# Performance work log

Measured on AMD Instinct MI355X. Metric: run time of the kernel, lower is better.

Reference implementation:

```python
import jax, jax.numpy as jnp
import numpy as np

H = 16        # num query heads
H_KV = 4      # num kv heads
D = 128       # head_dim
ROPE_BASE = 10000.0


def rotate_half(x):
    x1, x2 = jnp.split(x, 2, axis=-1)
    return jnp.concatenate((-x2, x1), axis=-1)


def rope_tables(T, d, dtype):
    inv_freq = 1.0 / (ROPE_BASE ** (np.arange(0, d, 2, dtype=np.float32) / d))
    t = np.arange(T, dtype=np.float32)
    freqs = np.outer(t, inv_freq)                 # [T, d/2]
    emb = np.concatenate((freqs, freqs), axis=-1)  # [T, d]
    return jnp.asarray(np.cos(emb), dtype), jnp.asarray(np.sin(emb), dtype)


def setup_inputs() -> dict:
    key = jax.random.key(0)
    ks = jax.random.split(key, 5)
    B, T, C = 2, 2048, 2048
    s = 0.02
    return {
        "x": jax.random.normal(ks[0], (B, T, C), jnp.float32),
        "wq": jax.random.normal(ks[1], (C, H * D), jnp.float32) * s,
        "wk": jax.random.normal(ks[2], (C, H_KV * D), jnp.float32) * s,
        "wv": jax.random.normal(ks[3], (C, H_KV * D), jnp.float32) * s,
        "wo": jax.random.normal(ks[4], (H * D, C), jnp.float32) * s,
    }


def reference(x, wq, wk, wv, wo):
    B, T, C = x.shape
    # QKV projections (bias=False); weights stored as [in, out]
    q = (x @ wq).reshape(B, T, H, D).transpose(0, 2, 1, 3)      # [B,H,T,D]
    k = (x @ wk).reshape(B, T, H_KV, D).transpose(0, 2, 1, 3)   # [B,Hkv,T,D]
    v = (x @ wv).reshape(B, T, H_KV, D).transpose(0, 2, 1, 3)
    # RoPE
    cos, sin = rope_tables(T, D, x.dtype)                        # [T,D]
    q = q * cos + rotate_half(q) * sin
    k = k * cos + rotate_half(k) * sin
    # GQA: repeat kv heads
    n_rep = H // H_KV
    k = jnp.repeat(k, n_rep, axis=1)                             # [B,H,T,D]
    v = jnp.repeat(v, n_rep, axis=1)
    # Causal SDPA
    scale = 1.0 / jnp.sqrt(jnp.asarray(D, x.dtype))
    att = jnp.einsum('bhqd,bhkd->bhqk', q, k) * scale            # [B,H,T,T]
    causal = jnp.tril(jnp.ones((T, T), dtype=bool))
    att = jnp.where(causal, att, jnp.asarray(-jnp.inf, x.dtype))
    att = jax.nn.softmax(att, axis=-1)
    y = jnp.einsum('bhqk,bhkd->bhqd', att, v)                    # [B,H,T,D]
    y = y.transpose(0, 2, 1, 3).reshape(B, T, H * D)
    return y @ wo
```

## Files before the change

kernel.cpp:

```cpp
#include <hip/hip_runtime.h>
#include <cstdint>
#include <cstddef>

typedef __attribute__((ext_vector_type(8))) short short8;
typedef __attribute__((ext_vector_type(4))) float f4;
typedef __attribute__((ext_vector_type(4))) unsigned int u4;

static __device__ __forceinline__ unsigned short f2bf(float x) {
  unsigned int u = __float_as_uint(x);
  unsigned int r = (u + 0x7FFFu + ((u >> 16) & 1u)) >> 16;
  return (unsigned short)r;
}

static __device__ __forceinline__ void gll16(const unsigned short* g, unsigned short* l) {
  __builtin_amdgcn_global_load_lds(
      (const __attribute__((address_space(1))) unsigned int*)g,
      (__attribute__((address_space(3))) unsigned int*)l, 16, 0, 0);
}

template <int N>
static __device__ __forceinline__ void wait_vmcnt() {
  if constexpr (N == 0) asm volatile("s_waitcnt vmcnt(0)" ::: "memory");
  else if constexpr (N == 1) asm volatile("s_waitcnt vmcnt(1)" ::: "memory");
  else if constexpr (N == 2) asm volatile("s_waitcnt vmcnt(2)" ::: "memory");
  else if constexpr (N == 3) asm volatile("s_waitcnt vmcnt(3)" ::: "memory");
  else if constexpr (N == 4) asm volatile("s_waitcnt vmcnt(4)" ::: "memory");
}

__global__ __launch_bounds__(256) void k_cvt(
    const float* __restrict__ src, unsigned short* __restrict__ dst) {
  int gid = blockIdx.x * 256 + threadIdx.x;
  const float* p = src + (size_t)gid * 8;
  f4 a = *(const f4*)p;
  f4 b = *(const f4*)(p + 4);
  union { unsigned short u[8]; u4 v; } pk;
#pragma unroll
  for (int i = 0; i < 4; ++i) { pk.u[i] = f2bf(a[i]); pk.u[4 + i] = f2bf(b[i]); }
  *(u4*)(dst + (size_t)gid * 8) = pk.v;
}

__global__ __launch_bounds__(256) void k_transpose_f(
    const float* __restrict__ src, unsigned short* __restrict__ dst, int R, int C) {
  __shared__ alignas(16) unsigned short tile[64 * 72];
  int tid = threadIdx.x;
  int c0 = blockIdx.x * 64, r0 = blockIdx.y * 64;
#pragma unroll
  for (int s = 0; s < 2; ++s) {
    int chunk = tid + s * 256;
    int c8 = chunk & 7, r = chunk >> 3;
    const float* p = src + (size_t)(r0 + r) * C + c0 + c8 * 8;
    f4 a = *(const f4*)p;
    f4 b = *(const f4*)(p + 4);
    union { unsigned short u[8]; u4 v; } pk;
#pragma unroll
    for (int i = 0; i < 4; ++i) { pk.u[i] = f2bf(a[i]); pk.u[4 + i] = f2bf(b[i]); }
    *(u4*)(tile + r * 72 + c8 * 8) = pk.v;
  }
  __syncthreads();
#pragma unroll
  for (int s = 0; s < 2; ++s) {
    int chunk = tid + s * 256;
    int r8 = chunk & 7, c = chunk >> 3;
    union { unsigned short u[8]; u4 v; } pk;
#pragma unroll
    for (int i = 0; i < 8; ++i) pk.u[i] = tile[(r8 * 8 + i) * 72 + c];
    *(u4*)(dst + (size_t)(c0 + c) * R + r0 + r8 * 8) = pk.v;
  }
}

#define PHASE(QM, QN, WAITC, ...)                                              \
  {                                                                            \
    wait_vmcnt<WAITC>();                                                       \
    __builtin_amdgcn_s_barrier();                                              \
    asm volatile("" ::: "memory");                                             \
    short8 af[FI][2], bf[2][2];                                                \
    _Pragma("unroll") for (int i = 0; i < FI; ++i)                             \
      _Pragma("unroll") for (int ks = 0; ks < 2; ++ks)                         \
        af[i][ks] = *(const short8*)(&As[cur][((QM) * (BM / 2) + wm * (BM / 4) + i * 16 + l16) * 64 + kswz[ks]]); \
    _Pragma("unroll") for (int j = 0; j < 2; ++j)                              \
      _Pragma("unroll") for (int ks = 0; ks < 2; ++ks)                         \
        bf[j][ks] = *(const short8*)(&Bs[cur][((QN) * 128 + wn * 32 + j * 16 + l16) * 64 + kswz[ks]]); \
    __VA_ARGS__                                                                \
    __builtin_amdgcn_s_setprio(1);                                             \
    _Pragma("unroll") for (int i = 0; i < FI; ++i)                             \
      _Pragma("unroll") for (int j = 0; j < 2; ++j)                            \
        _Pragma("unroll") for (int ks = 0; ks < 2; ++ks)                       \
          acc[(QM) * FI + i][(QN) * 2 + j] = __builtin_amdgcn_mfma_f32_16x16x32_bf16( \
              af[i][ks], bf[j][ks], acc[(QM) * FI + i][(QN) * 2 + j], 0, 0, 0); \
    __builtin_amdgcn_s_setprio(0);                                             \
  }

template <int BM, bool BF16OUT>
__global__ __launch_bounds__(512, 2) void k_gemm8(
    const unsigned short* __restrict__ A, const unsigned short* __restrict__ Bt,
    void* __restrict__ Cout, int M, int N, int K) {
  constexpr int CA = BM / 128;
  constexpr int FI = BM / 64;
  constexpr int WA = 2 + CA, WB = 2 * CA, WC = CA + 2, PB = CA;
  __shared__ alignas(16) unsigned short As[2][BM * 64];
  __shared__ alignas(16) unsigned short Bs[2][256 * 64];
  (void)M;

  int tid = threadIdx.x;
  int wid = tid >> 6, lane = tid & 63, quad = lane >> 4, l16 = lane & 15;
  int wm = wid >> 2, wn = wid & 3;

  int nx = gridDim.x;
  int id = blockIdx.y * nx + blockIdx.x;
  int nwg = nx * gridDim.y;
  int per = nwg >> 3;
  int lin = (id & 7) * per + (id >> 3);
  int bx = lin % nx, by = lin / nx;
  int bm = by * BM, bn = bx * 256;

  int srow = lane >> 3;
  int scol = ((lane & 7) ^ srow) << 3;
  const unsigned short* Ast = A + (size_t)(bm + wid * 8 + srow) * K + scol;
  const unsigned short* Bst = Bt + (size_t)(bn + wid * 8 + srow) * K + scol;
  const int ldsw = wid * 512;

  int kswz[2];
#pragma unroll
  for (int ks = 0; ks < 2; ++ks) kswz[ks] = (ks * 32 + quad * 8) ^ ((l16 & 7) << 3);

  f4 zero = {0.f, 0.f, 0.f, 0.f};
  f4 acc[2 * FI][4];
#pragma unroll
  for (int i = 0; i < 2 * FI; ++i)
#pragma unroll
    for (int j = 0; j < 4; ++j) acc[i][j] = zero;

  if constexpr (CA == 2) {
    gll16(Ast, &As[0][ldsw]);
    gll16(Ast + (size_t)64 * K, &As[0][ldsw + 64 * 64]);
  } else {
    gll16(Ast, &As[0][ldsw]);
  }
  gll16(Bst, &Bs[0][ldsw]);
  gll16(Bst + (size_t)64 * K, &Bs[0][ldsw + 64 * 64]);
  gll16(Bst + (size_t)128 * K, &Bs[0][ldsw + 128 * 64]);
  gll16(Bst + (size_t)192 * K, &Bs[0][ldsw + 192 * 64]);
  if constexpr (CA == 2) {
    gll16(Ast + (size_t)128 * K, &As[0][ldsw + 128 * 64]);
    gll16(Ast + (size_t)192 * K, &As[0][ldsw + 192 * 64]);
  } else {
    gll16(Ast + (size_t)64 * K, &As[0][ldsw + 64 * 64]);
  }

  int nt = K >> 6;
  int cur = 0;
  for (int t = 0; t < nt - 1; ++t) {
    int k0n = (t + 1) << 6;
    int nxt = cur ^ 1;
    unsigned short* Asn = &As[nxt][0];
    unsigned short* Bsn = &Bs[nxt][0];
    PHASE(0, 0, WA,
      if constexpr (CA == 2) {
        gll16(Ast + k0n, Asn + ldsw);
        gll16(Ast + (size_t)64 * K + k0n, Asn + ldsw + 64 * 64);
      } else {
        gll16(Ast + k0n, Asn + ldsw);
      })
    PHASE(0, 1, WB,
      gll16(Bst + k0n, Bsn + ldsw);
      gll16(Bst + (size_t)64 * K + k0n, Bsn + ldsw + 64 * 64);)
    PHASE(1, 0, WC,
      gll16(Bst + (size_t)128 * K + k0n, Bsn + ldsw + 128 * 64);
      gll16(Bst + (size_t)192 * K + k0n, Bsn + ldsw + 192 * 64);)
    PHASE(1, 1, -1,
      if constexpr (CA == 2) {
        gll16(Ast + (size_t)128 * K + k0n, Asn + ldsw + 128 * 64);
        gll16(Ast + (size_t)192 * K + k0n, Asn + ldsw + 192 * 64);
      } else {
        gll16(Ast + (size_t)64 * K + k0n, Asn + ldsw + 64 * 64);
      })
    cur = nxt;
  }
  PHASE(0, 0, WA, ;)
  PHASE(0, 1, PB, ;)
  PHASE(1, 0, 0, ;)
  PHASE(1, 1, -1, ;)

#pragma unroll
  for (int mi = 0; mi < 2 * FI; ++mi) {
    int row = bm + (mi / FI) * (BM / 2) + wm * (BM / 4) + (mi % FI) * 16 + quad * 4;
#pragma unroll
    for (int nj = 0; nj < 4; ++nj) {
      int col = bn + (nj >> 1) * 128 + wn * 32 + (nj & 1) * 16 + l16;
#pragma unroll
      for (int r = 0; r < 4; ++r) {
        if constexpr (BF16OUT)
          ((unsigned short*)Cout)[(size_t)(row + r) * N + col] = f2bf(acc[mi][nj][r]);
        else
          ((float*)Cout)[(size_t)(row + r) * N + col] = acc[mi][nj][r];
      }
    }
  }
}

__global__ __launch_bounds__(256) void k_rope(unsigned short* __restrict__ QKV) {
  int gid = blockIdx.x * 256 + threadIdx.x;
  const int TQ = 2 * 2048 * 16 * 64;
  bool isq = gid < TQ;
  int g = isq ? gid : gid - TQ;
  int d = g & 63; g >>= 6;
  int nh = isq ? 16 : 4;
  int h = g & (nh - 1); g >>= (isq ? 4 : 2);
  int t = g & 2047; int b = g >> 11;
  size_t p = (size_t)(b * 2048 + t) * 3072 + (isq ? 0 : 2048) + h * 128 + d;
  float x0 = __uint_as_float((unsigned int)QKV[p] << 16);
  float x1 = __uint_as_float((unsigned int)QKV[p + 64] << 16);
  float freq = exp2f(-(float)d * 0.20762050593046f);
  float ang = (float)t * freq;
  float cv = __cosf(ang), sv = __sinf(ang);
  float o0 = x0 * cv - x1 * sv;
  float o1 = x1 * cv + x0 * sv;
  if (isq) { o0 *= 0.088388347648318f; o1 *= 0.088388347648318f; }
  QKV[p] = f2bf(o0);
  QKV[p + 64] = f2bf(o1);
}

__global__ __launch_bounds__(256) void k_vtrans(
    const unsigned short* __restrict__ QKV, unsigned short* __restrict__ VT) {
  int gid = blockIdx.x * 256 + threadIdx.x;
  int t = gid & 2047; int g = gid >> 11;
  int d = g & 127; g >>= 7;
  int hk = g & 3; int b = g >> 2;
  VT[gid] = QKV[(size_t)(b * 2048 + t) * 3072 + 2560 + hk * 128 + d];
}

static __device__ __forceinline__ void attn_step(
    const unsigned short* __restrict__ Ks, const unsigned short* __restrict__ Vs,
    const short8* qf, f4* o, float& m, float& l,
    int quad, int l16, int qrow, int K0, bool mask) {
  f4 zero = {0.f, 0.f, 0.f, 0.f};
  f4 st[4];
#pragma unroll
  for (int kt = 0; kt < 4; ++kt) {
    st[kt] = zero;
#pragma unroll
    for (int ks = 0; ks < 4; ++ks) {
      short8 kf = *(const short8*)(Ks + (kt * 16 + l16) * 136 + ks * 32 + quad * 8);
      st[kt] = __builtin_amdgcn_mfma_f32_16x16x32_bf16(kf, qf[ks], st[kt], 0, 0, 0);
    }
  }
  if (mask) {
#pragma unroll
    for (int kt = 0; kt < 4; ++kt)
#pragma unroll
      for (int r = 0; r < 4; ++r)
        if (K0 + kt * 16 + quad * 4 + r > qrow) st[kt][r] = -1e30f;
  }
  float sm = -1e30f;
#pragma unroll
  for (int kt = 0; kt < 4; ++kt)
#pragma unroll
    for (int r = 0; r < 4; ++r) sm = fmaxf(sm, st[kt][r]);
  sm = fmaxf(sm, __shfl_xor(sm, 16));
  sm = fmaxf(sm, __shfl_xor(sm, 32));
  float mnew = fmaxf(m, sm);
  float alpha = __expf(m - mnew);
  f4 pv[4];
  float rs = 0.f;
#pragma unroll
  for (int kt = 0; kt < 4; ++kt)
#pragma unroll
    for (int r = 0; r < 4; ++r) {
      pv[kt][r] = __expf(st[kt][r] - mnew);
      rs += pv[kt][r];
    }
  rs += __shfl_xor(rs, 16);
  rs += __shfl_xor(rs, 32);
  l = l * alpha + rs;
  m = mnew;
#pragma unroll
  for (int i = 0; i < 8; ++i) o[i] *= alpha;
#pragma unroll
  for (int kh = 0; kh < 2; ++kh) {
    short8 pb;
#pragma unroll
    for (int j = 0; j < 8; ++j) {
      int srcl = (((quad * 2 + (j >> 2)) & 3) << 4) + l16;
      float va = __shfl(pv[kh * 2][j & 3], srcl);
      float vb = __shfl(pv[kh * 2 + 1][j & 3], srcl);
      pb[j] = (short)f2bf((quad >> 1) ? vb : va);
    }
#pragma unroll
    for (int i = 0; i < 8; ++i) {
      short8 vf = *(const short8*)(Vs + (i * 16 + l16) * 72 + kh * 32 + quad * 8);
      o[i] = __builtin_amdgcn_mfma_f32_16x16x32_bf16(vf, pb, o[i], 0, 0, 0);
    }
  }
}

__global__ __launch_bounds__(256, 2) void k_attn(
    const unsigned short* __restrict__ QKV,
    const unsigned short* __restrict__ VT,
    unsigned short* __restrict__ Y) {
  __shared__ alignas(16) unsigned short Ks[2][64 * 136];
  __shared__ alignas(16) unsigned short Vs[2][128 * 72];
  int tid = threadIdx.x;
  int w = tid >> 6, lane = tid & 63, quad = lane >> 4, l16 = lane & 15;
  int bh = blockIdx.y; int b = bh >> 4, h = bh & 15, hk = h >> 2;
  int v = blockIdx.x;
  int q0A = v * 64 + w * 16;
  int q0B = (31 - v) * 64 + w * 16;
  const unsigned short* Qh = QKV + (size_t)b * 2048 * 3072 + h * 128;
  const unsigned short* Kh = QKV + (size_t)b * 2048 * 3072 + 2048 + hk * 128;
  const unsigned short* Vh = VT + ((size_t)(b * 4 + hk) * 128) * 2048;

  int rK0 = tid >> 4, cK = tid & 15;
  int rV0 = tid >> 3, cV = tid & 7;

  short8 qfA[4], qfB[4];
#pragma unroll
  for (int ks = 0; ks < 4; ++ks) {
    qfA[ks] = *(const short8*)(Qh + (size_t)(q0A + l16) * 3072 + ks * 32 + quad * 8);
    qfB[ks] = *(const short8*)(Qh + (size_t)(q0B + l16) * 3072 + ks * 32 + quad * 8);
  }

  f4 zero = {0.f, 0.f, 0.f, 0.f};
  f4 oA[8], oB[8];
#pragma unroll
  for (int i = 0; i < 8; ++i) { oA[i] = zero; oB[i] = zero; }
  float mA = -1e30f, lA = 0.f, mB = -1e30f, lB = 0.f;

  int nch = 32 - v;

#pragma unroll
  for (int s = 0; s < 4; ++s) {
    int rK = rK0 + 16 * s;
    *(u4*)(&Ks[0][0] + rK * 136 + cK * 8) =
        *(const u4*)(Kh + (size_t)rK * 3072 + cK * 8);
    int rV = rV0 + 32 * s;
    *(u4*)(&Vs[0][0] + rV * 72 + cV * 8) =
        *(const u4*)(Vh + (size_t)rV * 2048 + cV * 8);
  }
  __syncthreads();

  for (int kc = 0; kc < nch; ++kc) {
    int cur = kc & 1, nxt = cur ^ 1;
    int K0 = kc * 64;
    bool have_next = (kc + 1) < nch;
    u4 kreg[4], vreg[4];
    if (have_next) {
      int K0n = K0 + 64;
#pragma unroll
      for (int s = 0; s < 4; ++s) {
        int rK = rK0 + 16 * s;
        kreg[s] = *(const u4*)(Kh + (size_t)(K0n + rK) * 3072 + cK * 8);
        int rV = rV0 + 32 * s;
        vreg[s] = *(const u4*)(Vh + (size_t)rV * 2048 + K0n + cV * 8);
      }
    }

    if (kc <= v)
      attn_step(&Ks[cur][0], &Vs[cur][0], qfA, oA, mA, lA, quad, l16, q0A + l16, K0, kc == v);
    attn_step(&Ks[cur][0], &Vs[cur][0], qfB, oB, mB, lB, quad, l16, q0B + l16, K0, kc == nch - 1);

    if (have_next) {
#pragma unroll
      for (int s = 0; s < 4; ++s) {
        int rK = rK0 + 16 * s;
        *(u4*)(&Ks[nxt][0] + rK * 136 + cK * 8) = kreg[s];
        int rV = rV0 + 32 * s;
        *(u4*)(&Vs[nxt][0] + rV * 72 + cV * 8) = vreg[s];
      }
    }
    __syncthreads();
  }

  float rA = 1.f / lA, rB = 1.f / lB;
  size_t yrowA = (size_t)(b * 2048 + q0A + l16) * 2048 + h * 128;
  size_t yrowB = (size_t)(b * 2048 + q0B + l16) * 2048 + h * 128;
#pragma unroll
  for (int i = 0; i < 8; ++i)
#pragma unroll
    for (int r = 0; r < 4; ++r) {
      Y[yrowA + i * 16 + quad * 4 + r] = f2bf(oA[i][r] * rA);
      Y[yrowB + i * 16 + quad * 4 + r] = f2bf(oB[i][r] * rB);
    }
}

extern "C" void kernel_launch(void* const* d_in, const int* in_sizes, int n_in,
                              void* d_out, int out_size, void* d_ws, size_t ws_size,
                              hipStream_t stream) {
  const float* x  = (const float*)d_in[0];
  const float* wq = (const float*)d_in[1];
  const float* wk = (const float*)d_in[2];
  const float* wv = (const float*)d_in[3];
  const float* wo = (const float*)d_in[4];
  float* outp = (float*)d_out;

  unsigned short* WqkvT = (unsigned short*)d_out;
  unsigned short* VT    = WqkvT + (size_t)3072 * 2048;
  unsigned short* Xb    = VT + (size_t)2 * 4 * 128 * 2048;
  unsigned short* QKV = (unsigned short*)d_ws;
  unsigned short* Yb  = QKV + (size_t)4096 * 3072;
  unsigned short* WoT = QKV;

  dim3 blk(256);
  k_cvt<<<dim3(4096), blk, 0, stream>>>(x, Xb);
  k_transpose_f<<<dim3(32, 32), blk, 0, stream>>>(wq, WqkvT, 2048, 2048);
  k_transpose_f<<<dim3(8, 32), blk, 0, stream>>>(wk, WqkvT + (size_t)2048 * 2048, 2048, 512);
  k_transpose_f<<<dim3(8, 32), blk, 0, stream>>>(wv, WqkvT + (size_t)2560 * 2048, 2048, 512);

  k_gemm8<256, true><<<dim3(12, 16), dim3(512), 0, stream>>>(
      Xb, WqkvT, QKV, 4096, 3072, 2048);

  k_rope<<<dim3(20480), blk, 0, stream>>>(QKV);
  k_vtrans<<<dim3(8192), blk, 0, stream>>>(QKV, VT);

  k_attn<<<dim3(16, 32), blk, 0, stream>>>(QKV, VT, Yb);

  k_transpose_f<<<dim3(32, 32), blk, 0, stream>>>(wo, WoT, 2048, 2048);
  k_gemm8<128, false><<<dim3(8, 32), dim3(512), 0, stream>>>(
      Yb, WoT, outp, 4096, 2048, 2048);
}
```

Before: 337.4 us.

## Vectorize RoPE and V-transpose, add lazy softmax rescale and permlane P repack

```diff
diff --git a/kernel.cpp b/kernel.cpp
--- a/kernel.cpp
+++ b/kernel.cpp
@@ -198,41 +198,68 @@
   }
 }
 
-__global__ __launch_bounds__(256) void k_rope(unsigned short* __restrict__ QKV) {
+__global__ __launch_bounds__(256) void k_rope8(unsigned short* __restrict__ QKV) {
   int gid = blockIdx.x * 256 + threadIdx.x;
-  const int TQ = 2 * 2048 * 16 * 64;
-  bool isq = gid < TQ;
-  int g = isq ? gid : gid - TQ;
-  int d = g & 63; g >>= 6;
-  int nh = isq ? 16 : 4;
-  int h = g & (nh - 1); g >>= (isq ? 4 : 2);
+  int c8 = gid & 7; int g = gid >> 3;
+  int h20 = g % 20; g /= 20;
   int t = g & 2047; int b = g >> 11;
-  size_t p = (size_t)(b * 2048 + t) * 3072 + (isq ? 0 : 2048) + h * 128 + d;
-  float x0 = __uint_as_float((unsigned int)QKV[p] << 16);
-  float x1 = __uint_as_float((unsigned int)QKV[p + 64] << 16);
-  float freq = exp2f(-(float)d * 0.20762050593046f);
-  float ang = (float)t * freq;
-  float cv = __cosf(ang), sv = __sinf(ang);
-  float o0 = x0 * cv - x1 * sv;
-  float o1 = x1 * cv + x0 * sv;
-  if (isq) { o0 *= 0.088388347648318f; o1 *= 0.088388347648318f; }
-  QKV[p] = f2bf(o0);
-  QKV[p + 64] = f2bf(o1);
-}
-
-__global__ __launch_bounds__(256) void k_vtrans(
+  bool isq = h20 < 16;
+  size_t p = (size_t)(b * 2048 + t) * 3072 +
+             (isq ? h20 * 128 : 2048 + (h20 - 16) * 128) + c8 * 8;
+  short8 x0 = *(const short8*)(QKV + p);
+  short8 x1 = *(const short8*)(QKV + p + 64);
+  short8 o0, o1;
+  float tf = (float)t;
+#pragma unroll
+  for (int i = 0; i < 8; ++i) {
+    int d = c8 * 8 + i;
+    float a0 = __uint_as_float((unsigned int)(unsigned short)x0[i] << 16);
+    float a1 = __uint_as_float((unsigned int)(unsigned short)x1[i] << 16);
+    float freq = exp2f(-(float)d * 0.20762050593046f);
+    float ang = tf * freq;
+    float cv = __cosf(ang), sv = __sinf(ang);
+    float r0 = a0 * cv - a1 * sv;
+    float r1 = a1 * cv + a0 * sv;
+    if (isq) { r0 *= 0.088388347648318f; r1 *= 0.088388347648318f; }
+    o0[i] = (short)f2bf(r0);
+    o1[i] = (short)f2bf(r1);
+  }
+  *(short8*)(QKV + p) = o0;
+  *(short8*)(QKV + p + 64) = o1;
+}
+
+__global__ __launch_bounds__(256) void k_vtrans2(
     const unsigned short* __restrict__ QKV, unsigned short* __restrict__ VT) {
-  int gid = blockIdx.x * 256 + threadIdx.x;
-  int t = gid & 2047; int g = gid >> 11;
-  int d = g & 127; g >>= 7;
-  int hk = g & 3; int b = g >> 2;
-  VT[gid] = QKV[(size_t)(b * 2048 + t) * 3072 + 2560 + hk * 128 + d];
+  __shared__ alignas(16) unsigned short tile[64 * 72];
+  int tid = threadIdx.x;
+  int t0 = blockIdx.x * 64;
+  int g = blockIdx.y;
+  int dh = g & 1, hk = (g >> 1) & 3, b = g >> 3;
+  int d0 = dh * 64;
+  const unsigned short* src = QKV + (size_t)(b * 2048 + t0) * 3072 + 2560 + hk * 128 + d0;
+#pragma unroll
+  for (int s = 0; s < 2; ++s) {
+    int chunk = tid + s * 256;
+    int c8 = chunk & 7, r = chunk >> 3;
+    *(u4*)(tile + r * 72 + c8 * 8) = *(const u4*)(src + (size_t)r * 3072 + c8 * 8);
+  }
+  __syncthreads();
+  unsigned short* dst = VT + ((size_t)((b * 4 + hk) * 128 + d0)) * 2048 + t0;
+#pragma unroll
+  for (int s = 0; s < 2; ++s) {
+    int chunk = tid + s * 256;
+    int r8 = chunk & 7, c = chunk >> 3;
+    union { unsigned short u[8]; u4 v; } pk;
+#pragma unroll
+    for (int i = 0; i < 8; ++i) pk.u[i] = tile[(r8 * 8 + i) * 72 + c];
+    *(u4*)(dst + (size_t)c * 2048 + r8 * 8) = pk.v;
+  }
 }
 
 static __device__ __forceinline__ void attn_step(
     const unsigned short* __restrict__ Ks, const unsigned short* __restrict__ Vs,
     const short8* qf, f4* o, float& m, float& l,
-    int quad, int l16, int qrow, int K0, bool mask) {
+    int quad, int l16, int qrow, int K0, bool mask, bool odd) {
   f4 zero = {0.f, 0.f, 0.f, 0.f};
   f4 st[4];
 #pragma unroll
@@ -258,8 +285,8 @@
     for (int r = 0; r < 4; ++r) sm = fmaxf(sm, st[kt][r]);
   sm = fmaxf(sm, __shfl_xor(sm, 16));
   sm = fmaxf(sm, __shfl_xor(sm, 32));
-  float mnew = fmaxf(m, sm);
-  float alpha = __expf(m - mnew);
+  bool grow = !__all(sm - m <= 8.f);
+  float mnew = grow ? fmaxf(m, sm) : m;
   f4 pv[4];
   float rs = 0.f;
 #pragma unroll
@@ -271,24 +298,41 @@
     }
   rs += __shfl_xor(rs, 16);
   rs += __shfl_xor(rs, 32);
-  l = l * alpha + rs;
-  m = mnew;
-#pragma unroll
-  for (int i = 0; i < 8; ++i) o[i] *= alpha;
+  if (grow) {
+    float alpha = __expf(m - mnew);
+    l = l * alpha + rs;
+    m = mnew;
+#pragma unroll
+    for (int i = 0; i < 8; ++i) o[i] *= alpha;
+  } else {
+    l += rs;
+  }
+  unsigned int c[4][2];
+#pragma unroll
+  for (int kt = 0; kt < 4; ++kt)
+#pragma unroll
+    for (int p = 0; p < 2; ++p)
+      asm("v_cvt_pk_bf16_f32 %0, %1, %2"
+          : "=v"(c[kt][p]) : "v"(pv[kt][2 * p]), "v"(pv[kt][2 * p + 1]));
 #pragma unroll
   for (int kh = 0; kh < 2; ++kh) {
-    short8 pb;
-#pragma unroll
-    for (int j = 0; j < 8; ++j) {
-      int srcl = (((quad * 2 + (j >> 2)) & 3) << 4) + l16;
-      float va = __shfl(pv[kh * 2][j & 3], srcl);
-      float vb = __shfl(pv[kh * 2 + 1][j & 3], srcl);
-      pb[j] = (short)f2bf((quad >> 1) ? vb : va);
-    }
+    unsigned int A0 = c[2 * kh][0], A1 = c[2 * kh][1];
+    unsigned int B0 = c[2 * kh + 1][0], B1 = c[2 * kh + 1][1];
+    asm("v_permlane32_swap_b32 %0, %1" : "+v"(A0), "+v"(B0));
+    asm("v_permlane32_swap_b32 %0, %1" : "+v"(A1), "+v"(B1));
+    unsigned int tA0 = (unsigned int)__builtin_amdgcn_ds_swizzle((int)A0, 0x401F);
+    unsigned int tA1 = (unsigned int)__builtin_amdgcn_ds_swizzle((int)A1, 0x401F);
+    unsigned int tB0 = (unsigned int)__builtin_amdgcn_ds_swizzle((int)B0, 0x401F);
+    unsigned int tB1 = (unsigned int)__builtin_amdgcn_ds_swizzle((int)B1, 0x401F);
+    union { unsigned int u[4]; short8 s; } pb;
+    pb.u[0] = odd ? tB0 : A0;
+    pb.u[1] = odd ? tB1 : A1;
+    pb.u[2] = odd ? B0 : tA0;
+    pb.u[3] = odd ? B1 : tA1;
 #pragma unroll
     for (int i = 0; i < 8; ++i) {
       short8 vf = *(const short8*)(Vs + (i * 16 + l16) * 72 + kh * 32 + quad * 8);
-      o[i] = __builtin_amdgcn_mfma_f32_16x16x32_bf16(vf, pb, o[i], 0, 0, 0);
+      o[i] = __builtin_amdgcn_mfma_f32_16x16x32_bf16(vf, pb.s, o[i], 0, 0, 0);
     }
   }
 }
@@ -301,6 +345,7 @@
   __shared__ alignas(16) unsigned short Vs[2][128 * 72];
   int tid = threadIdx.x;
   int w = tid >> 6, lane = tid & 63, quad = lane >> 4, l16 = lane & 15;
+  bool odd = (quad & 1) != 0;
   int bh = blockIdx.y; int b = bh >> 4, h = bh & 15, hk = h >> 2;
   int v = blockIdx.x;
   int q0A = v * 64 + w * 16;
@@ -355,8 +400,8 @@
     }
 
     if (kc <= v)
-      attn_step(&Ks[cur][0], &Vs[cur][0], qfA, oA, mA, lA, quad, l16, q0A + l16, K0, kc == v);
-    attn_step(&Ks[cur][0], &Vs[cur][0], qfB, oB, mB, lB, quad, l16, q0B + l16, K0, kc == nch - 1);
+      attn_step(&Ks[cur][0], &Vs[cur][0], qfA, oA, mA, lA, quad, l16, q0A + l16, K0, kc == v, odd);
+    attn_step(&Ks[cur][0], &Vs[cur][0], qfB, oB, mB, lB, quad, l16, q0B + l16, K0, kc == nch - 1, odd);
 
     if (have_next) {
 #pragma unroll
@@ -408,8 +453,8 @@
   k_gemm8<256, true><<<dim3(12, 16), dim3(512), 0, stream>>>(
       Xb, WqkvT, QKV, 4096, 3072, 2048);
 
-  k_rope<<<dim3(20480), blk, 0, stream>>>(QKV);
-  k_vtrans<<<dim3(8192), blk, 0, stream>>>(QKV, VT);
+  k_rope8<<<dim3(2560), blk, 0, stream>>>(QKV);
+  k_vtrans2<<<dim3(32, 16), blk, 0, stream>>>(QKV, VT);
 
   k_attn<<<dim3(16, 32), blk, 0, stream>>>(QKV, VT, Yb);
 
```

Result: faster. 310.0 us (-8.1%).
